# Kernel tuning notes

Hardware: AMD Instinct MI355X
Metric: run time of the kernel (lower is better)

Reference implementation:

```python
import jax, jax.numpy as jnp
import numpy as np

EMB_DIM = 512
REDUCED_DIM = 64


def setup_inputs() -> dict:
    key = jax.random.key(0)
    k1, k2, k3 = jax.random.split(key, 3)
    B, K1, K2 = 8, 2048, 2048
    embeddings_a = jax.random.normal(k1, (B, K1, EMB_DIM), dtype=jnp.float32)
    embeddings_b = jax.random.normal(k2, (B, K2, EMB_DIM), dtype=jnp.float32)
    # learned params (random_normal init in keras defaults to stddev=0.05)
    R = jax.random.normal(k3, (EMB_DIM, REDUCED_DIM), dtype=jnp.float32) * 0.05
    b = jnp.full((1,), -3.0, dtype=jnp.float32)
    return {"embeddings_a": embeddings_a, "embeddings_b": embeddings_b, "R": R, "b": b}


def reference(embeddings_a, embeddings_b, R, b):
    # inference mode: dropout is identity
    emb_scale = 1.0 / np.float32(np.sqrt(R.shape[0]))      # 1/sqrt(embedding_dim)
    red_scale = 1.0 / np.float32(np.sqrt(R.shape[1]))      # 1/sqrt(reduced_dim)
    ra = jnp.matmul(embeddings_a, R) * emb_scale            # (B, k1, r)
    rb = jnp.matmul(embeddings_b, R) * emb_scale            # (B, k2, r)
    scores = jnp.einsum('bkr,blr->bkl', ra, rb) * red_scale # (B, k1, k2)
    scores = scores + b
    # mask columns where the full embedding_b vector is zero (padding)
    mask = jnp.all(embeddings_b == 0, axis=-1)              # (B, k2)
    scores = scores - 1e9 * mask[:, None, :].astype(scores.dtype)
    return jax.nn.softmax(scores, axis=-1)
```

## Files before the change

kernel.cpp:

```cpp
#include <hip/hip_runtime.h>
#include <hip/hip_bf16.h>

#define EMB 512
#define RD  64
#define NB  8
#define K1  2048
#define K2  2048

typedef short bf16x8 __attribute__((ext_vector_type(8)));
typedef float f32x4  __attribute__((ext_vector_type(4)));

#define SCALE_B 0.04419417382415922f
#define SCALE_A 0.005524271728019902f

__global__ __launch_bounds__(256) void k_prep_rt(
    const float* __restrict__ R, __hip_bfloat16* __restrict__ Rt)
{
  int idx = blockIdx.x * 256 + threadIdx.x;
  int k = idx >> 6, n = idx & 63;
  Rt[(size_t)n * EMB + k] = __float2bfloat16(R[idx]);
}

__global__ __launch_bounds__(256) void k_project(
    const float* __restrict__ A, const float* __restrict__ Bm,
    const __hip_bfloat16* __restrict__ Rt,
    __hip_bfloat16* __restrict__ ra, __hip_bfloat16* __restrict__ rb,
    unsigned char* __restrict__ mask)
{
  const int t = threadIdx.x;
  const int w = t >> 6, lane = t & 63;
  const int m = lane & 15, quad = lane >> 4;
  const int blk = blockIdx.x;
  const bool isB = blk >= 256;
  const float* __restrict__ src = isB ? Bm : A;
  const int rowbase = ((isB ? blk - 256 : blk) * 4 + w) * 16;
  const float* __restrict__ xrow = src + (size_t)(rowbase + m) * EMB;

  f32x4 acc[4] = {{0.f,0.f,0.f,0.f},{0.f,0.f,0.f,0.f},
                  {0.f,0.f,0.f,0.f},{0.f,0.f,0.f,0.f}};
  float nzm = 0.f;

  #pragma unroll
  for (int kk = 0; kk < EMB; kk += 32) {
    float4 x0 = *reinterpret_cast<const float4*>(xrow + kk + quad * 8);
    float4 x1 = *reinterpret_cast<const float4*>(xrow + kk + quad * 8 + 4);

    nzm = fmaxf(nzm, fmaxf(fmaxf(fabsf(x0.x), fabsf(x0.y)),
                           fmaxf(fabsf(x0.z), fabsf(x0.w))));
    nzm = fmaxf(nzm, fmaxf(fmaxf(fabsf(x1.x), fabsf(x1.y)),
                           fmaxf(fabsf(x1.z), fabsf(x1.w))));

    union { bf16x8 v; __hip_bfloat16 h[8]; } af;
    af.h[0] = __float2bfloat16(x0.x); af.h[1] = __float2bfloat16(x0.y);
    af.h[2] = __float2bfloat16(x0.z); af.h[3] = __float2bfloat16(x0.w);
    af.h[4] = __float2bfloat16(x1.x); af.h[5] = __float2bfloat16(x1.y);
    af.h[6] = __float2bfloat16(x1.z); af.h[7] = __float2bfloat16(x1.w);

    #pragma unroll
    for (int nt = 0; nt < 4; ++nt) {
      bf16x8 bf = *reinterpret_cast<const bf16x8*>(
          Rt + (size_t)(nt * 16 + m) * EMB + kk + quad * 8);
      acc[nt] = __builtin_amdgcn_mfma_f32_16x16x32_bf16(af.v, bf, acc[nt], 0, 0, 0);
    }
  }

  const float scale = isB ? SCALE_B : SCALE_A;
  __hip_bfloat16* __restrict__ dst = isB ? rb : ra;
  #pragma unroll
  for (int nt = 0; nt < 4; ++nt) {
    #pragma unroll
    for (int i = 0; i < 4; ++i) {
      const int r = rowbase + quad * 4 + i;
      dst[(size_t)r * RD + nt * 16 + m] = __float2bfloat16(acc[nt][i] * scale);
    }
  }

  float v = nzm;
  v = fmaxf(v, __shfl_xor(v, 16));
  v = fmaxf(v, __shfl_xor(v, 32));
  if (isB && lane < 16)
    mask[rowbase + lane] = (v == 0.f) ? 1 : 0;
}

__global__ __launch_bounds__(256) void k_scores(
    const __hip_bfloat16* __restrict__ ra, const __hip_bfloat16* __restrict__ rb,
    const unsigned char* __restrict__ mask, const float* __restrict__ bptr,
    float* __restrict__ out)
{
  const int bz = blockIdx.y;
  const int row_base = blockIdx.x * 16;
  const int w = threadIdx.x >> 6, lane = threadIdx.x & 63;
  const int m = lane & 15, quad = lane >> 4;
  const float bias = bptr[0];

  const __hip_bfloat16* __restrict__ raB = ra + ((size_t)bz * K1 + row_base) * RD;
  const __hip_bfloat16* __restrict__ rbB = rb + (size_t)bz * K2 * RD;
  const unsigned char* __restrict__ mk = mask + bz * K2;

  bf16x8 a0 = *reinterpret_cast<const bf16x8*>(raB + m * RD + quad * 8);
  bf16x8 a1 = *reinterpret_cast<const bf16x8*>(raB + m * RD + 32 + quad * 8);

  float e[32][4];
  float sums[4] = {0.f, 0.f, 0.f, 0.f};

  #pragma unroll
  for (int it = 0; it < 32; ++it) {
    const int tle = it * 4 + w;
    const int n = tle * 16 + m;
    bf16x8 b0 = *reinterpret_cast<const bf16x8*>(rbB + n * RD + quad * 8);
    bf16x8 b1 = *reinterpret_cast<const bf16x8*>(rbB + n * RD + 32 + quad * 8);
    f32x4 c = {0.f, 0.f, 0.f, 0.f};
    c = __builtin_amdgcn_mfma_f32_16x16x32_bf16(a0, b0, c, 0, 0, 0);
    c = __builtin_amdgcn_mfma_f32_16x16x32_bf16(a1, b1, c, 0, 0, 0);
    const bool msk = mk[n] != 0;
    #pragma unroll
    for (int i = 0; i < 4; ++i) {
      float v = msk ? 0.f : __expf(c[i] + bias);
      e[it][i] = v;
      sums[i] += v;
    }
  }

  #pragma unroll
  for (int i = 0; i < 4; ++i) {
    float v = sums[i];
    v += __shfl_xor(v, 1);
    v += __shfl_xor(v, 2);
    v += __shfl_xor(v, 4);
    v += __shfl_xor(v, 8);
    sums[i] = v;
  }

  __shared__ float partial[4][16];
  __shared__ float rowinv[16];
  if ((lane & 15) == 0) {
    #pragma unroll
    for (int i = 0; i < 4; ++i) partial[w][quad * 4 + i] = sums[i];
  }
  __syncthreads();
  if (threadIdx.x < 16) {
    float tsum = partial[0][threadIdx.x] + partial[1][threadIdx.x] +
                 partial[2][threadIdx.x] + partial[3][threadIdx.x];
    rowinv[threadIdx.x] = 1.0f / tsum;
  }
  __syncthreads();

  float inv[4];
  #pragma unroll
  for (int i = 0; i < 4; ++i) inv[i] = rowinv[quad * 4 + i];

  float* __restrict__ outB = out + ((size_t)bz * K1 + row_base) * K2;
  #pragma unroll
  for (int it = 0; it < 32; ++it) {
    const int n = (it * 4 + w) * 16 + m;
    #pragma unroll
    for (int i = 0; i < 4; ++i)
      outB[(size_t)(quad * 4 + i) * K2 + n] = e[it][i] * inv[i];
  }
}

extern "C" void kernel_launch(void* const* d_in, const int* in_sizes, int n_in,
                              void* d_out, int out_size, void* d_ws, size_t ws_size,
                              hipStream_t stream) {
  const float* A  = (const float*)d_in[0];
  const float* Bm = (const float*)d_in[1];
  const float* R  = (const float*)d_in[2];
  const float* bb = (const float*)d_in[3];
  float* out = (float*)d_out;

  char* ws = (char*)d_ws;
  __hip_bfloat16* ra  = (__hip_bfloat16*)(ws);
  __hip_bfloat16* rb  = (__hip_bfloat16*)(ws + (((size_t)2) << 20));
  __hip_bfloat16* Rt  = (__hip_bfloat16*)(ws + (((size_t)4) << 20));
  unsigned char*  msk = (unsigned char*) (ws + (((size_t)4) << 20) + 65536);

  k_prep_rt<<<dim3(128), dim3(256), 0, stream>>>(R, Rt);
  k_project<<<dim3(512), dim3(256), 0, stream>>>(A, Bm, Rt, ra, rb, msk);
  k_scores <<<dim3(K1 / 16, NB), dim3(256), 0, stream>>>(ra, rb, msk, bb, out);
}
```

Before: 241.4 us.

## Pack softmax exponentials to bf16 pairs, prefetch projection loads, coalesce Rt prep

The scores kernel now keeps its cached exponentials as bf16 pairs packed into 32-bit registers instead of 128 float registers, and processes two column tiles per iteration to interleave the MFMAs. This halves register pressure, which should allow higher occupancy and more memory-level parallelism. The projection kernel software-prefetches the next float4 pair of input rows, and the R transpose kernel now writes coalesced instead of reading coalesced. The risk is that the output probabilities are rounded to bf16 before normalization, which loses precision and may fail tolerance.

```diff
diff --git a/kernel.cpp b/kernel.cpp
--- a/kernel.cpp
+++ b/kernel.cpp
@@ -13,12 +13,22 @@
 #define SCALE_B 0.04419417382415922f
 #define SCALE_A 0.005524271728019902f
 
+__device__ __forceinline__ float bf16lo_to_f(unsigned int u) {
+  union { unsigned int u; float f; } c; c.u = u << 16; return c.f;
+}
+__device__ __forceinline__ float bf16hi_to_f(unsigned int u) {
+  union { unsigned int u; float f; } c; c.u = u & 0xFFFF0000u; return c.f;
+}
+__device__ __forceinline__ unsigned short f_to_bf16u(float v) {
+  union { __hip_bfloat16 h; unsigned short s; } c; c.h = __float2bfloat16(v); return c.s;
+}
+
 __global__ __launch_bounds__(256) void k_prep_rt(
     const float* __restrict__ R, __hip_bfloat16* __restrict__ Rt)
 {
   int idx = blockIdx.x * 256 + threadIdx.x;
-  int k = idx >> 6, n = idx & 63;
-  Rt[(size_t)n * EMB + k] = __float2bfloat16(R[idx]);
+  int n = idx >> 9, k = idx & 511;
+  Rt[idx] = __float2bfloat16(R[(size_t)k * RD + n]);
 }
 
 __global__ __launch_bounds__(256) void k_project(
@@ -34,16 +44,19 @@
   const bool isB = blk >= 256;
   const float* __restrict__ src = isB ? Bm : A;
   const int rowbase = ((isB ? blk - 256 : blk) * 4 + w) * 16;
-  const float* __restrict__ xrow = src + (size_t)(rowbase + m) * EMB;
+  const float4* __restrict__ xp =
+      reinterpret_cast<const float4*>(src + (size_t)(rowbase + m) * EMB) + quad * 2;
 
   f32x4 acc[4] = {{0.f,0.f,0.f,0.f},{0.f,0.f,0.f,0.f},
                   {0.f,0.f,0.f,0.f},{0.f,0.f,0.f,0.f}};
   float nzm = 0.f;
 
-  #pragma unroll
-  for (int kk = 0; kk < EMB; kk += 32) {
-    float4 x0 = *reinterpret_cast<const float4*>(xrow + kk + quad * 8);
-    float4 x1 = *reinterpret_cast<const float4*>(xrow + kk + quad * 8 + 4);
+  float4 x0 = xp[0], x1 = xp[1];
+
+  #pragma unroll
+  for (int s = 0; s < 16; ++s) {
+    float4 p0, p1;
+    if (s < 15) { p0 = xp[(s + 1) * 8]; p1 = xp[(s + 1) * 8 + 1]; }
 
     nzm = fmaxf(nzm, fmaxf(fmaxf(fabsf(x0.x), fabsf(x0.y)),
                            fmaxf(fabsf(x0.z), fabsf(x0.w))));
@@ -56,12 +69,14 @@
     af.h[4] = __float2bfloat16(x1.x); af.h[5] = __float2bfloat16(x1.y);
     af.h[6] = __float2bfloat16(x1.z); af.h[7] = __float2bfloat16(x1.w);
 
+    const int kk = s * 32;
     #pragma unroll
     for (int nt = 0; nt < 4; ++nt) {
       bf16x8 bf = *reinterpret_cast<const bf16x8*>(
           Rt + (size_t)(nt * 16 + m) * EMB + kk + quad * 8);
       acc[nt] = __builtin_amdgcn_mfma_f32_16x16x32_bf16(af.v, bf, acc[nt], 0, 0, 0);
     }
+    x0 = p0; x1 = p1;
   }
 
   const float scale = isB ? SCALE_B : SCALE_A;
@@ -100,24 +115,30 @@
   bf16x8 a0 = *reinterpret_cast<const bf16x8*>(raB + m * RD + quad * 8);
   bf16x8 a1 = *reinterpret_cast<const bf16x8*>(raB + m * RD + 32 + quad * 8);
 
-  float e[32][4];
+  unsigned int epk[16][4];
   float sums[4] = {0.f, 0.f, 0.f, 0.f};
 
   #pragma unroll
-  for (int it = 0; it < 32; ++it) {
-    const int tle = it * 4 + w;
-    const int n = tle * 16 + m;
-    bf16x8 b0 = *reinterpret_cast<const bf16x8*>(rbB + n * RD + quad * 8);
-    bf16x8 b1 = *reinterpret_cast<const bf16x8*>(rbB + n * RD + 32 + quad * 8);
-    f32x4 c = {0.f, 0.f, 0.f, 0.f};
-    c = __builtin_amdgcn_mfma_f32_16x16x32_bf16(a0, b0, c, 0, 0, 0);
-    c = __builtin_amdgcn_mfma_f32_16x16x32_bf16(a1, b1, c, 0, 0, 0);
-    const bool msk = mk[n] != 0;
+  for (int it2 = 0; it2 < 16; ++it2) {
+    const int n0 = (it2 * 8 + w) * 16 + m;
+    const int n1 = (it2 * 8 + 4 + w) * 16 + m;
+    bf16x8 b00 = *reinterpret_cast<const bf16x8*>(rbB + n0 * RD + quad * 8);
+    bf16x8 b01 = *reinterpret_cast<const bf16x8*>(rbB + n0 * RD + 32 + quad * 8);
+    bf16x8 b10 = *reinterpret_cast<const bf16x8*>(rbB + n1 * RD + quad * 8);
+    bf16x8 b11 = *reinterpret_cast<const bf16x8*>(rbB + n1 * RD + 32 + quad * 8);
+    f32x4 c0 = {0.f, 0.f, 0.f, 0.f}, c1 = {0.f, 0.f, 0.f, 0.f};
+    c0 = __builtin_amdgcn_mfma_f32_16x16x32_bf16(a0, b00, c0, 0, 0, 0);
+    c1 = __builtin_amdgcn_mfma_f32_16x16x32_bf16(a0, b10, c1, 0, 0, 0);
+    c0 = __builtin_amdgcn_mfma_f32_16x16x32_bf16(a1, b01, c0, 0, 0, 0);
+    c1 = __builtin_amdgcn_mfma_f32_16x16x32_bf16(a1, b11, c1, 0, 0, 0);
+    const bool k0 = mk[n0] != 0, k1 = mk[n1] != 0;
     #pragma unroll
     for (int i = 0; i < 4; ++i) {
-      float v = msk ? 0.f : __expf(c[i] + bias);
-      e[it][i] = v;
-      sums[i] += v;
+      float v0 = k0 ? 0.f : __expf(c0[i] + bias);
+      float v1 = k1 ? 0.f : __expf(c1[i] + bias);
+      sums[i] += v0 + v1;
+      epk[it2][i] = (unsigned int)f_to_bf16u(v0) |
+                    ((unsigned int)f_to_bf16u(v1) << 16);
     }
   }
 
@@ -151,11 +172,15 @@
 
   float* __restrict__ outB = out + ((size_t)bz * K1 + row_base) * K2;
   #pragma unroll
-  for (int it = 0; it < 32; ++it) {
-    const int n = (it * 4 + w) * 16 + m;
-    #pragma unroll
-    for (int i = 0; i < 4; ++i)
-      outB[(size_t)(quad * 4 + i) * K2 + n] = e[it][i] * inv[i];
+  for (int it2 = 0; it2 < 16; ++it2) {
+    const int n0 = (it2 * 8 + w) * 16 + m;
+    const int n1 = (it2 * 8 + 4 + w) * 16 + m;
+    #pragma unroll
+    for (int i = 0; i < 4; ++i) {
+      const size_t rowoff = (size_t)(quad * 4 + i) * K2;
+      outB[rowoff + n0] = bf16lo_to_f(epk[it2][i]) * inv[i];
+      outB[rowoff + n1] = bf16hi_to_f(epk[it2][i]) * inv[i];
+    }
   }
 }
 
```

Result: faster. 222.3 us (-7.9%).
